# Kernel tuning notes

Hardware: AMD Instinct MI355X
Metric: run time of the kernel (lower is better)

The kernel has to match this reference:

```python
import jax, jax.numpy as jnp
import numpy as np

D_MODEL = 1536
N_HEADS = 16
HEAD_DIM = D_MODEL // N_HEADS  # 96
NUM_BLOCKS = HEAD_DIM // 24    # 4


def generate_leech_kernel(dim=24):
    base = np.zeros((dim, dim), dtype=np.float32)
    for i in range(dim - 1):
        base[i, i] = 2.0
        base[i, i + 1] = 2.0
    base[-1, -1] = 2.0
    base[-1, 0] = -2.0
    q, _ = np.linalg.qr(base)
    return jnp.asarray(q.astype(np.float32))


def setup_inputs() -> dict:
    key = jax.random.key(0)
    k1, k2, k3 = jax.random.split(key, 3)
    x = jax.random.normal(k1, (2, 2048, D_MODEL), dtype=jnp.float32)
    # nn.Linear weights stored [out, in]; kept that layout, applied as x @ W.T
    w_qkv = jax.random.normal(k2, (3 * D_MODEL, D_MODEL), dtype=jnp.float32) * (D_MODEL ** -0.5)
    w_out = jax.random.normal(k3, (D_MODEL, D_MODEL), dtype=jnp.float32) * (D_MODEL ** -0.5)
    leech_kernel = generate_leech_kernel(24)
    return {"x": x, "w_qkv": w_qkv, "w_out": w_out, "leech_kernel": leech_kernel}


def _apply_kernel(t, kernel):
    # t: [b, h, s, head_dim] -> blockwise 24x24 rotation
    b, h, s, d = t.shape
    t = t.reshape(b, h, s, NUM_BLOCKS, 24)
    t = jnp.einsum('bhsni,ij->bhsnj', t, kernel)
    return t.reshape(b, h, s, d)


def reference(x, w_qkv, w_out, leech_kernel):
    bsz, steps, _ = x.shape
    qkv = x @ w_qkv.T  # [b, s, 3*d]
    qkv = qkv.reshape(bsz, steps, 3, N_HEADS, HEAD_DIM)
    qkv = jnp.transpose(qkv, (2, 0, 3, 1, 4))  # [3, b, h, s, hd]
    q, k, v = qkv[0], qkv[1], qkv[2]
    q = _apply_kernel(q, leech_kernel)
    k = _apply_kernel(k, leech_kernel)
    scale = HEAD_DIM ** -0.5
    scores = jnp.einsum('bhqd,bhkd->bhqk', q, k) * scale
    attn = jax.nn.softmax(scores, axis=-1)
    out = jnp.einsum('bhqk,bhkd->bhqd', attn, v)
    out = jnp.transpose(out, (0, 2, 1, 3)).reshape(bsz, steps, -1)
    return out @ w_out.T
```

## Files before the change

kernel.cpp:

```cpp
#include <hip/hip_runtime.h>
#include <cmath>

#define D_MODEL 1536
#define N_HEADS 16
#define HEAD_DIM 96
#define SEQ 2048
#define BATCH 2
#define M_TOTAL 4096
#define N_QKV 4608
#define QK_LOG2E 0.14724449f

typedef unsigned short ushort_t;
typedef __attribute__((ext_vector_type(8))) short bf16x8;
typedef __attribute__((ext_vector_type(4))) float f32x4;

static __device__ __forceinline__ ushort_t f2bf(float f) {
    unsigned u = __builtin_bit_cast(unsigned, f);
    u += 0x7fffu + ((u >> 16) & 1u);
    return (ushort_t)(u >> 16);
}

static __device__ __forceinline__ unsigned pk2bf(float lo, float hi) {
#if __has_builtin(__builtin_amdgcn_cvt_pk_bf16_f32)
    auto v = __builtin_amdgcn_cvt_pk_bf16_f32(lo, hi);
    return __builtin_bit_cast(unsigned, v);
#else
    return (unsigned)f2bf(lo) | ((unsigned)f2bf(hi) << 16);
#endif
}

static __device__ __forceinline__ float fast_exp2(float x) {
#if __has_builtin(__builtin_amdgcn_exp2f)
    return __builtin_amdgcn_exp2f(x);
#else
    return __expf(x * 0.69314718056f);
#endif
}

typedef const __attribute__((address_space(1))) unsigned int* gas_t;
typedef __attribute__((address_space(3))) unsigned int* las_t;
static __device__ __forceinline__ void gld_lds16(const void* g, void* l) {
    __builtin_amdgcn_global_load_lds((gas_t)g, (las_t)l, 16, 0, 0);
}

#define MFMA16(a, b, c) __builtin_amdgcn_mfma_f32_16x16x32_bf16(a, b, c, 0, 0, 0)

__global__ __launch_bounds__(256) void convert_f32_bf16(
    const float* __restrict__ in, ushort_t* __restrict__ out, int n)
{
    const int i = (blockIdx.x * 256 + threadIdx.x) * 4;
    if (i >= n) return;
    float4 v = *(const float4*)(in + i);
    ushort4 o;
    o.x = f2bf(v.x); o.y = f2bf(v.y); o.z = f2bf(v.z); o.w = f2bf(v.w);
    *(ushort4*)(out + i) = o;
}

__global__ __launch_bounds__(256) void prep_wqkv(
    const float* __restrict__ W, const float* __restrict__ Kern,
    ushort_t* __restrict__ Wb)
{
    __shared__ float Kl[576];
    const int t = threadIdx.x;
    for (int i = t; i < 576; i += 256) Kl[i] = Kern[i];
    __syncthreads();
    const int g = blockIdx.y;
    const int k = blockIdx.x * 256 + t;
    const float* src = W + (size_t)g * 24 * D_MODEL + k;
    ushort_t* dst = Wb + (size_t)g * 24 * D_MODEL + k;
    if (g < 128) {
        float in[24];
#pragma unroll
        for (int i = 0; i < 24; ++i) in[i] = src[(size_t)i * D_MODEL];
#pragma unroll
        for (int j = 0; j < 24; ++j) {
            float s = 0.f;
#pragma unroll
            for (int i = 0; i < 24; ++i) s = fmaf(in[i], Kl[i * 24 + j], s);
            dst[(size_t)j * D_MODEL] = f2bf(s);
        }
    } else {
#pragma unroll
        for (int i = 0; i < 24; ++i) dst[(size_t)i * D_MODEL] = f2bf(src[(size_t)i * D_MODEL]);
    }
}

__global__ __launch_bounds__(256, 4) void gemm_qkv_bf16(
    const ushort_t* __restrict__ X, const ushort_t* __restrict__ W,
    ushort_t* __restrict__ qb, ushort_t* __restrict__ kb, ushort_t* __restrict__ vtb)
{
    __shared__ ushort_t As[128 * 64];
    __shared__ ushort_t Bs[128 * 64];
    const int t = threadIdx.x;
    const int lane = t & 63, w = t >> 6;
    const int c = lane & 15, qd = lane >> 4;
    const int m0 = blockIdx.y * 128, n0 = blockIdx.x * 128;
    const int wr = (w >> 1) * 64, wc = (w & 1) * 64;
    const int lr = lane >> 3;
    const int lc = (lane & 7) ^ lr;
    const char* Xb = (const char*)X;
    const char* Wp = (const char*)W;
    const size_t rowb = 2 * D_MODEL;

    f32x4 acc[4][4];
#pragma unroll
    for (int i = 0; i < 4; ++i)
#pragma unroll
        for (int j = 0; j < 4; ++j) acc[i][j] = {0.f, 0.f, 0.f, 0.f};

    for (int k0 = 0; k0 < D_MODEL; k0 += 64) {
        __syncthreads();
#pragma unroll
        for (int j = 0; j < 4; ++j) {
            const int g = w * 4 + j;
            const int row = g * 8 + lr;
            gld_lds16(Xb + (size_t)(m0 + row) * rowb + k0 * 2 + lc * 16,
                      (char*)As + g * 1024);
            gld_lds16(Wp + (size_t)(n0 + row) * rowb + k0 * 2 + lc * 16,
                      (char*)Bs + g * 1024);
        }
        __syncthreads();
#pragma unroll
        for (int kc = 0; kc < 2; ++kc) {
            const int sx = ((kc * 4 + qd) ^ (c & 7)) * 16;
            bf16x8 af[4], bfr[4];
#pragma unroll
            for (int i = 0; i < 4; ++i)
                af[i] = *(const bf16x8*)((const char*)As + (wr + i * 16 + c) * 128 + sx);
#pragma unroll
            for (int j = 0; j < 4; ++j)
                bfr[j] = *(const bf16x8*)((const char*)Bs + (wc + j * 16 + c) * 128 + sx);
#pragma unroll
            for (int i = 0; i < 4; ++i)
#pragma unroll
                for (int j = 0; j < 4; ++j)
                    acc[i][j] = MFMA16(af[i], bfr[j], acc[i][j]);
        }
    }
#pragma unroll
    for (int j = 0; j < 4; ++j) {
        const int n = n0 + wc + j * 16 + c;
        const int which = n / D_MODEL;
        const int rem = n % D_MODEL;
        const int head = rem / HEAD_DIM;
        const int d = rem % HEAD_DIM;
        if (which < 2) {
            ushort_t* dst = which == 0 ? qb : kb;
            const float sc2 = which == 0 ? QK_LOG2E : 1.0f;
#pragma unroll
            for (int i = 0; i < 4; ++i)
#pragma unroll
                for (int r = 0; r < 4; ++r) {
                    const int m = m0 + wr + i * 16 + qd * 4 + r;
                    const int b_ = m >> 11, s_ = m & (SEQ - 1);
                    dst[((size_t)(b_ * N_HEADS + head) * SEQ + s_) * HEAD_DIM + d] =
                        f2bf(acc[i][j][r] * sc2);
                }
        } else {
            const int b_ = m0 >> 11;
            const int sb = (m0 & (SEQ - 1)) + wr + qd * 4;
            ushort_t* dstv = vtb + ((size_t)(b_ * N_HEADS + head) * HEAD_DIM + d) * SEQ;
#pragma unroll
            for (int i = 0; i < 4; ++i) {
                ushort4 o4;
                o4.x = f2bf(acc[i][j][0]); o4.y = f2bf(acc[i][j][1]);
                o4.z = f2bf(acc[i][j][2]); o4.w = f2bf(acc[i][j][3]);
                *(ushort4*)&dstv[sb + i * 16] = o4;
            }
        }
    }
}

__global__ __launch_bounds__(256, 4) void gemm_out_bf16(
    const ushort_t* __restrict__ A, const ushort_t* __restrict__ W,
    float* __restrict__ C)
{
    __shared__ ushort_t As[128 * 64];
    __shared__ ushort_t Bs[128 * 64];
    const int t = threadIdx.x;
    const int lane = t & 63, w = t >> 6;
    const int c = lane & 15, qd = lane >> 4;
    const int m0 = blockIdx.y * 128, n0 = blockIdx.x * 128;
    const int wr = (w >> 1) * 64, wc = (w & 1) * 64;
    const int lr = lane >> 3;
    const int lc = (lane & 7) ^ lr;
    const char* Ab = (const char*)A;
    const char* Wp = (const char*)W;
    const size_t rowb = 2 * D_MODEL;

    f32x4 acc[4][4];
#pragma unroll
    for (int i = 0; i < 4; ++i)
#pragma unroll
        for (int j = 0; j < 4; ++j) acc[i][j] = {0.f, 0.f, 0.f, 0.f};

    for (int k0 = 0; k0 < D_MODEL; k0 += 64) {
        __syncthreads();
#pragma unroll
        for (int j = 0; j < 4; ++j) {
            const int g = w * 4 + j;
            const int row = g * 8 + lr;
            gld_lds16(Ab + (size_t)(m0 + row) * rowb + k0 * 2 + lc * 16,
                      (char*)As + g * 1024);
            gld_lds16(Wp + (size_t)(n0 + row) * rowb + k0 * 2 + lc * 16,
                      (char*)Bs + g * 1024);
        }
        __syncthreads();
#pragma unroll
        for (int kc = 0; kc < 2; ++kc) {
            const int sx = ((kc * 4 + qd) ^ (c & 7)) * 16;
            bf16x8 af[4], bfr[4];
#pragma unroll
            for (int i = 0; i < 4; ++i)
                af[i] = *(const bf16x8*)((const char*)As + (wr + i * 16 + c) * 128 + sx);
#pragma unroll
            for (int j = 0; j < 4; ++j)
                bfr[j] = *(const bf16x8*)((const char*)Bs + (wc + j * 16 + c) * 128 + sx);
#pragma unroll
            for (int i = 0; i < 4; ++i)
#pragma unroll
                for (int j = 0; j < 4; ++j)
                    acc[i][j] = MFMA16(af[i], bfr[j], acc[i][j]);
        }
    }
#pragma unroll
    for (int i = 0; i < 4; ++i)
#pragma unroll
        for (int j = 0; j < 4; ++j)
#pragma unroll
            for (int r = 0; r < 4; ++r)
                C[(size_t)(m0 + wr + i * 16 + qd * 4 + r) * D_MODEL + n0 + wc + j * 16 + c] =
                    acc[i][j][r];
}

__global__ __launch_bounds__(256, 3) void flash_bf16(
    const ushort_t* __restrict__ Q, const ushort_t* __restrict__ K,
    const ushort_t* __restrict__ VT, ushort_t* __restrict__ attn)
{
    __shared__ ushort_t Ks[12 * 64 * 8];
    __shared__ ushort_t Vt[96 * 64];
    __shared__ ushort_t Ps[4][32 * 72];

    const int t = threadIdx.x;
    const int lane = t & 63, w = t >> 6;
    const int c = lane & 15, qd = lane >> 4;
    const int lr = lane >> 3;
    const int lc = (lane & 7) ^ lr;
    const int h = blockIdx.y, bb = blockIdx.z;
    const int q0 = blockIdx.x * 128;
    const size_t base = ((size_t)(bb * N_HEADS + h)) * SEQ * HEAD_DIM;
    const ushort_t* Qb = Q + base;
    const char* Kb = (const char*)(K + base);
    const ushort_t* VTb = VT + base;

    bf16x8 aq[2][3];
#pragma unroll
    for (int qi = 0; qi < 2; ++qi)
#pragma unroll
        for (int kc = 0; kc < 3; ++kc)
            aq[qi][kc] = *(const bf16x8*)(Qb +
                (size_t)(q0 + w * 32 + qi * 16 + c) * HEAD_DIM + kc * 32 + qd * 8);

    f32x4 oacc[6][2];
#pragma unroll
    for (int jd = 0; jd < 6; ++jd)
#pragma unroll
        for (int qi = 0; qi < 2; ++qi) oacc[jd][qi] = {0.f, 0.f, 0.f, 0.f};
    float lrow[2] = {0.f, 0.f};

    for (int kt = 0; kt < SEQ / 64; ++kt) {
        __syncthreads();
        {
            const char* kp = Kb + (size_t)kt * 64 * 192;
#pragma unroll
            for (int jj = 0; jj < 3; ++jj) {
                const int g = w * 3 + jj;
                gld_lds16(kp + (size_t)lane * 192 + g * 16, (char*)Ks + g * 1024);
            }
        }
#pragma unroll
        for (int jj = 0; jj < 3; ++jj) {
            const int g = w * 3 + jj;
            const int d = g * 8 + lr;
            gld_lds16((const char*)(VTb + (size_t)d * SEQ + kt * 64 + lc * 8),
                      (char*)Vt + g * 1024);
        }
        __syncthreads();

        f32x4 sacc[4][2];
#pragma unroll
        for (int kti = 0; kti < 4; ++kti)
#pragma unroll
            for (int qi = 0; qi < 2; ++qi) sacc[kti][qi] = {0.f, 0.f, 0.f, 0.f};
#pragma unroll
        for (int kc = 0; kc < 3; ++kc) {
            bf16x8 ak[4];
#pragma unroll
            for (int kti = 0; kti < 4; ++kti)
                ak[kti] = *(const bf16x8*)&Ks[((kc * 4 + qd) * 64 + kti * 16 + c) * 8];
#pragma unroll
            for (int kti = 0; kti < 4; ++kti)
#pragma unroll
                for (int qi = 0; qi < 2; ++qi)
                    sacc[kti][qi] = MFMA16(ak[kti], aq[qi][kc], sacc[kti][qi]);
        }

        float ls0 = 0.f, ls1 = 0.f;
#pragma unroll
        for (int kti = 0; kti < 4; ++kti)
#pragma unroll
            for (int qi = 0; qi < 2; ++qi) {
                const float p0 = fast_exp2(sacc[kti][qi][0]);
                const float p1 = fast_exp2(sacc[kti][qi][1]);
                const float p2 = fast_exp2(sacc[kti][qi][2]);
                const float p3 = fast_exp2(sacc[kti][qi][3]);
                uint2 pk;
                pk.x = pk2bf(p0, p1);
                pk.y = pk2bf(p2, p3);
                *(uint2*)&Ps[w][(qi * 16 + c) * 72 + kti * 16 + qd * 4] = pk;
                const float s = (p0 + p1) + (p2 + p3);
                if (qi == 0) ls0 += s; else ls1 += s;
            }
        ls0 += __shfl_xor(ls0, 16, 64); ls0 += __shfl_xor(ls0, 32, 64);
        ls1 += __shfl_xor(ls1, 16, 64); ls1 += __shfl_xor(ls1, 32, 64);
        lrow[0] += ls0; lrow[1] += ls1;

#pragma unroll
        for (int kc = 0; kc < 2; ++kc) {
            bf16x8 bp[2];
#pragma unroll
            for (int qi = 0; qi < 2; ++qi)
                bp[qi] = *(const bf16x8*)&Ps[w][(qi * 16 + c) * 72 + kc * 32 + qd * 8];
#pragma unroll
            for (int jd = 0; jd < 6; ++jd) {
                const int sx = ((kc * 4 + qd) ^ (c & 7)) * 16;
                const bf16x8 av =
                    *(const bf16x8*)((const char*)Vt + (jd * 16 + c) * 128 + sx);
#pragma unroll
                for (int qi = 0; qi < 2; ++qi)
                    oacc[jd][qi] = MFMA16(av, bp[qi], oacc[jd][qi]);
            }
        }
    }

#pragma unroll
    for (int qi = 0; qi < 2; ++qi) {
        const float linv = 1.0f / lrow[qi];
        const int row = bb * SEQ + q0 + w * 32 + qi * 16 + c;
        ushort_t* dst = attn + (size_t)row * D_MODEL + h * HEAD_DIM + qd * 4;
#pragma unroll
        for (int jd = 0; jd < 6; ++jd) {
            ushort4 o4;
            o4.x = f2bf(oacc[jd][qi][0] * linv);
            o4.y = f2bf(oacc[jd][qi][1] * linv);
            o4.z = f2bf(oacc[jd][qi][2] * linv);
            o4.w = f2bf(oacc[jd][qi][3] * linv);
            *(ushort4*)(dst + jd * 16) = o4;
        }
    }
}


extern "C" void kernel_launch(void* const* d_in, const int* in_sizes, int n_in,
                              void* d_out, int out_size, void* d_ws, size_t ws_size,
                              hipStream_t stream)
{
    const float* x     = (const float*)d_in[0];
    const float* w_qkv = (const float*)d_in[1];
    const float* w_out = (const float*)d_in[2];
    const float* leech = (const float*)d_in[3];
    float* out = (float*)d_out;
    char* ws = (char*)d_ws;

    ushort_t* xb    = (ushort_t*)(ws);
    ushort_t* wqkvb = (ushort_t*)(ws + 12582912);
    ushort_t* woutb = (ushort_t*)(ws + 26738688);
    ushort_t* qb    = (ushort_t*)(ws + 31457280);
    ushort_t* kb    = (ushort_t*)(ws + 44040192);
    ushort_t* vtb   = (ushort_t*)(ws + 56623104);
    ushort_t* attnb = (ushort_t*)(ws + 69206016);

    convert_f32_bf16<<<6144, 256, 0, stream>>>(x, xb, M_TOTAL * D_MODEL);
    prep_wqkv<<<dim3(6, 192), 256, 0, stream>>>(w_qkv, leech, wqkvb);
    convert_f32_bf16<<<2304, 256, 0, stream>>>(w_out, woutb, D_MODEL * D_MODEL);

    gemm_qkv_bf16<<<dim3(N_QKV / 128, M_TOTAL / 128), 256, 0, stream>>>(
        xb, wqkvb, qb, kb, vtb);

    flash_bf16<<<dim3(SEQ / 128, N_HEADS, BATCH), 256, 0, stream>>>(
        qb, kb, vtb, attnb);

    gemm_out_bf16<<<dim3(D_MODEL / 128, M_TOTAL / 128), 256, 0, stream>>>(
        attnb, woutb, out);
}
```

Before: 282.8 us.

## Double-buffer K and V^T tiles in the flash attention kernel

Splits the shared-memory K and V^T tiles into two buffers. The asynchronous global-to-LDS loads for the next key tile are issued before the current tile is computed, so load latency can overlap with the MFMA and exp work. This also removes one barrier per iteration. The cost is roughly double the LDS for K and V, so launch bounds drop from 3 to 2 blocks per SM, which may reduce latency hiding across waves. The overlap only holds if the compiler does not insert a conservative vmcnt wait before the LDS reads of the current buffer.

```diff
diff --git a/kernel.cpp b/kernel.cpp
--- a/kernel.cpp
+++ b/kernel.cpp
@@ -233,12 +233,12 @@
                     acc[i][j][r];
 }
 
-__global__ __launch_bounds__(256, 3) void flash_bf16(
+__global__ __launch_bounds__(256, 2) void flash_bf16(
     const ushort_t* __restrict__ Q, const ushort_t* __restrict__ K,
     const ushort_t* __restrict__ VT, ushort_t* __restrict__ attn)
 {
-    __shared__ ushort_t Ks[12 * 64 * 8];
-    __shared__ ushort_t Vt[96 * 64];
+    __shared__ ushort_t Ks[2][12 * 64 * 8];
+    __shared__ ushort_t Vt[2][96 * 64];
     __shared__ ushort_t Ps[4][32 * 72];
 
     const int t = threadIdx.x;
@@ -268,24 +268,30 @@
         for (int qi = 0; qi < 2; ++qi) oacc[jd][qi] = {0.f, 0.f, 0.f, 0.f};
     float lrow[2] = {0.f, 0.f};
 
+    const int g0 = w * 3;
+#define ISSUE_STAGE(buf, ktv)                                                   \
+    {                                                                           \
+        const char* kp = Kb + (size_t)(ktv) * 64 * 192;                         \
+        _Pragma("unroll")                                                       \
+        for (int jj = 0; jj < 3; ++jj) {                                        \
+            const int g = g0 + jj;                                              \
+            gld_lds16(kp + (size_t)lane * 192 + g * 16, (char*)Ks[buf] + g * 1024); \
+        }                                                                       \
+        _Pragma("unroll")                                                       \
+        for (int jj = 0; jj < 3; ++jj) {                                        \
+            const int g = g0 + jj;                                              \
+            const int d = g * 8 + lr;                                           \
+            gld_lds16((const char*)(VTb + (size_t)d * SEQ + (ktv) * 64 + lc * 8), \
+                      (char*)Vt[buf] + g * 1024);                               \
+        }                                                                       \
+    }
+
+    ISSUE_STAGE(0, 0)
+
     for (int kt = 0; kt < SEQ / 64; ++kt) {
+        const int cur = kt & 1;
         __syncthreads();
-        {
-            const char* kp = Kb + (size_t)kt * 64 * 192;
-#pragma unroll
-            for (int jj = 0; jj < 3; ++jj) {
-                const int g = w * 3 + jj;
-                gld_lds16(kp + (size_t)lane * 192 + g * 16, (char*)Ks + g * 1024);
-            }
-        }
-#pragma unroll
-        for (int jj = 0; jj < 3; ++jj) {
-            const int g = w * 3 + jj;
-            const int d = g * 8 + lr;
-            gld_lds16((const char*)(VTb + (size_t)d * SEQ + kt * 64 + lc * 8),
-                      (char*)Vt + g * 1024);
-        }
-        __syncthreads();
+        if (kt + 1 < SEQ / 64) ISSUE_STAGE(cur ^ 1, kt + 1)
 
         f32x4 sacc[4][2];
 #pragma unroll
@@ -297,7 +303,7 @@
             bf16x8 ak[4];
 #pragma unroll
             for (int kti = 0; kti < 4; ++kti)
-                ak[kti] = *(const bf16x8*)&Ks[((kc * 4 + qd) * 64 + kti * 16 + c) * 8];
+                ak[kti] = *(const bf16x8*)&Ks[cur][((kc * 4 + qd) * 64 + kti * 16 + c) * 8];
 #pragma unroll
             for (int kti = 0; kti < 4; ++kti)
 #pragma unroll
@@ -335,13 +341,14 @@
             for (int jd = 0; jd < 6; ++jd) {
                 const int sx = ((kc * 4 + qd) ^ (c & 7)) * 16;
                 const bf16x8 av =
-                    *(const bf16x8*)((const char*)Vt + (jd * 16 + c) * 128 + sx);
+                    *(const bf16x8*)((const char*)Vt[cur] + (jd * 16 + c) * 128 + sx);
 #pragma unroll
                 for (int qi = 0; qi < 2; ++qi)
                     oacc[jd][qi] = MFMA16(av, bp[qi], oacc[jd][qi]);
             }
         }
     }
+#undef ISSUE_STAGE
 
 #pragma unroll
     for (int qi = 0; qi < 2; ++qi) {
```

Result: slower. 293.4 us (+3.8%).
